# Optimization experiments

Hardware: AMD Instinct MI355X
Metric: run time of the kernel (lower is better)

Reference implementation:

```python
import jax, jax.numpy as jnp
import numpy as np

B, T, F, H = 512, 365, 16, 256


def _lstm_layer(x, W_ih, W_hh, b_ih, b_hh):
    """batch_first LSTM layer, torch gate order (i, f, g, o).
    x: [B, T, in]. Returns (outputs [B, T, H], final h [B, H])."""
    # Precompute input projections for all timesteps: [T, B, 4H]
    x_proj = jnp.einsum('bti,gi->tbg', x, W_ih) + (b_ih + b_hh)
    h0 = jnp.zeros((x.shape[0], W_hh.shape[1]), x.dtype)
    c0 = jnp.zeros_like(h0)

    def step(carry, xp):
        h, c = carry
        z = xp + h @ W_hh.T  # [B, 4H]
        i, f, g, o = jnp.split(z, 4, axis=-1)
        c = jax.nn.sigmoid(f) * c + jax.nn.sigmoid(i) * jnp.tanh(g)
        h = jax.nn.sigmoid(o) * jnp.tanh(c)
        return (h, c), h

    (hT, _), hs = jax.lax.scan(step, (h0, c0), x_proj)
    return jnp.transpose(hs, (1, 0, 2)), hT


def setup_inputs() -> dict:
    key = jax.random.key(0)
    ks = jax.random.split(key, 11)
    s1 = 1.0 / np.sqrt(H)
    u = lambda k, shape: jax.random.uniform(k, shape, jnp.float32, -s1, s1)
    return {
        'x': jax.random.normal(ks[0], (B, T, F), jnp.float32),
        'W_ih1': u(ks[1], (4 * H, F)),
        'W_hh1': u(ks[2], (4 * H, H)),
        'b_ih1': u(ks[3], (4 * H,)),
        'b_hh1': u(ks[4], (4 * H,)),
        'W_ih2': u(ks[5], (4 * H, H)),
        'W_hh2': u(ks[6], (4 * H, H)),
        'b_ih2': u(ks[7], (4 * H,)),
        'b_hh2': u(ks[8], (4 * H,)),
        'W_lin': u(ks[9], (1, H)),
        'b_lin': u(ks[10], (1,)),
    }


def reference(x, W_ih1, W_hh1, b_ih1, b_hh1, W_ih2, W_hh2, b_ih2, b_hh2, W_lin, b_lin):
    h1_seq, _ = _lstm_layer(x, W_ih1, W_hh1, b_ih1, b_hh1)
    # dropout(p=0.1) is identity in eval mode
    _, hT = _lstm_layer(h1_seq, W_ih2, W_hh2, b_ih2, b_hh2)
    out = (hT @ W_lin.T + b_lin).reshape(-1)  # [B]
    return out
```

## Files before the change

kernel.cpp:

```cpp
#include <hip/hip_runtime.h>


#define T_STEPS 365
#define RS 564

typedef __attribute__((ext_vector_type(8))) short short8;
typedef __attribute__((ext_vector_type(4))) float float4_;
typedef __attribute__((ext_vector_type(4))) unsigned int uint4_;
typedef unsigned long long u64;
typedef unsigned int u32;

#define MFMA16(a, b, c) __builtin_amdgcn_mfma_f32_16x16x32_bf16((a), (b), (c), 0, 0, 0)

__device__ __forceinline__ unsigned short f2bf(float v) {
    union { float f; u32 u; } a; a.f = v;
    u32 r = a.u + 0x7fffu + ((a.u >> 16) & 1u);
    return (unsigned short)(r >> 16);
}
__device__ __forceinline__ float bf2f(unsigned short h) {
    union { u32 u; float f; } a; a.u = ((u32)h) << 16; return a.f;
}
__device__ __forceinline__ u32 packhl(float v) {
    unsigned short hi = f2bf(v);
    unsigned short lo = f2bf(v - bf2f(hi));
    return ((u32)hi << 16) | (u32)lo;
}
__device__ __forceinline__ float sigm(float x)  { return 1.f / (1.f + __expf(-x)); }
__device__ __forceinline__ float tanh_(float x) { return 2.f / (1.f + __expf(-2.f * x)) - 1.f; }

__device__ __forceinline__ void unpk(uint4_ a, uint4_ b, short8& hi, short8& lo) {
    union U { u32 d[4]; short8 s; } H, L;
    H.d[0] = __builtin_amdgcn_perm(a.y, a.x, 0x07060302u);
    H.d[1] = __builtin_amdgcn_perm(a.w, a.z, 0x07060302u);
    H.d[2] = __builtin_amdgcn_perm(b.y, b.x, 0x07060302u);
    H.d[3] = __builtin_amdgcn_perm(b.w, b.z, 0x07060302u);
    L.d[0] = __builtin_amdgcn_perm(a.y, a.x, 0x05040100u);
    L.d[1] = __builtin_amdgcn_perm(a.w, a.z, 0x05040100u);
    L.d[2] = __builtin_amdgcn_perm(b.y, b.x, 0x05040100u);
    L.d[3] = __builtin_amdgcn_perm(b.w, b.z, 0x05040100u);
    hi = H.s; lo = L.s;
}

__global__ void prep_w(
    const float* __restrict__ Wih1, const float* __restrict__ Whh1,
    const float* __restrict__ bih1, const float* __restrict__ bhh1,
    const float* __restrict__ Wih2, const float* __restrict__ Whh2,
    const float* __restrict__ bih2, const float* __restrict__ bhh2,
    unsigned short* __restrict__ w1h, unsigned short* __restrict__ w1l,
    unsigned short* __restrict__ w2h, unsigned short* __restrict__ w2l,
    float* __restrict__ bias1, float* __restrict__ bias2)
{
    const int tile = blockIdx.x;
    const int g = tile >> 4, ns = tile & 15;
    const int tid = threadIdx.x;

    for (int idx = tid; idx < 9 * 512; idx += 256) {
        int ks = idx >> 9, off = idx & 511, r = off >> 5, kk = off & 31;
        int R = g * 256 + ns * 16 + r;
        float v;
        if (ks < 8)       v = Whh1[R * 256 + ks * 32 + kk];
        else if (kk < 16) v = Wih1[R * 16 + kk];
        else              v = 0.f;
        unsigned short h = f2bf(v);
        size_t d = (size_t)(tile * 9 + ks) * 512 + off;
        w1h[d] = h; w1l[d] = f2bf(v - bf2f(h));
    }
    for (int idx = tid; idx < 16 * 512; idx += 256) {
        int ks = idx >> 9, off = idx & 511, r = off >> 5, kk = off & 31;
        int R = g * 256 + ns * 16 + r;
        int k = ks * 32 + kk;
        float v = (k < 256) ? Wih2[R * 256 + k] : Whh2[R * 256 + (k - 256)];
        unsigned short h = f2bf(v);
        size_t d = (size_t)(tile * 16 + ks) * 512 + off;
        w2h[d] = h; w2l[d] = f2bf(v - bf2f(h));
    }
    if (tid < 16) {
        int R = g * 256 + ns * 16 + tid;
        bias1[R] = bih1[R] + bhh1[R];
        bias2[R] = bih2[R] + bhh2[R];
    }
}

__global__ __launch_bounds__(512, 2) void lstm_main(
    const float* __restrict__ x,
    const unsigned short* __restrict__ w1h, const unsigned short* __restrict__ w1l,
    const unsigned short* __restrict__ w2h, const unsigned short* __restrict__ w2l,
    const float* __restrict__ bias1, const float* __restrict__ bias2,
    u32* hb1, u32* hb2, u32* prog,
    const float* __restrict__ Wlin, const float* __restrict__ blin,
    float* __restrict__ out)
{
    __shared__ __align__(16) u32 A2u[32 * RS];
    __shared__ __align__(16) float zb1[3 * 64 * 36];
    __shared__ __align__(16) float zb2[5 * 64 * 36];
    __shared__ __align__(16) float hp[32][17];
    __shared__ u32 rdy;

    const int tid  = threadIdx.x;
    const int lane = tid & 63;
    const int wv   = tid >> 6;
    const int quad = lane >> 4;
    const int r16  = lane & 15;
    const int bg   = blockIdx.x & 15;
    const int ns   = blockIdx.x >> 4;

    u32* myprog = prog + bg * 256;

    const bool isL1 = (wv < 3);
    int t0, t1_, t2_, t3_;
    if      (wv == 0) { t0 = 0;  t1_ = 1;  t2_ = 2;  t3_ = -1; }
    else if (wv == 1) { t0 = 3;  t1_ = 4;  t2_ = 5;  t3_ = -1; }
    else if (wv == 2) { t0 = 6;  t1_ = 7;  t2_ = 8;  t3_ = -1; }
    else if (wv == 3) { t0 = 0;  t1_ = 1;  t2_ = 2;  t3_ = 3;  }
    else if (wv == 4) { t0 = 4;  t1_ = 5;  t2_ = 6;  t3_ = -1; }
    else if (wv == 5) { t0 = 7;  t1_ = 9;  t2_ = 10; t3_ = -1; }
    else if (wv == 6) { t0 = 11; t1_ = 12; t2_ = 13; t3_ = -1; }
    else              { t0 = 14; t1_ = 15; t2_ = 16; t3_ = -1; }

    const int loff = r16 * 32 + quad * 8;
    const unsigned short* WHsrc = isL1 ? w1h : w2h;
    const unsigned short* WLsrc = isL1 ? w1l : w2l;
    const int NK = isL1 ? 9 : 16;
    short8 WH[4][4], WL[4][4];
#pragma unroll
    for (int s = 0; s < 4; s++) {
        const int b = (s == 0) ? t0 : (s == 1) ? t1_ : (s == 2) ? t2_ : t3_;
#pragma unroll
        for (int g = 0; g < 4; g++) {
            if (b >= 0) {
                int ks = (!isL1 && b > 8) ? (b - 1) : b;
                size_t off = ((size_t)((g * 16 + ns) * NK + ks)) * 512 + loff;
                WH[g][s] = *(const short8*)(WHsrc + off);
                WL[g][s] = *(const short8*)(WLsrc + off);
            } else {
                WH[g][s] = short8{0,0,0,0,0,0,0,0};
                WL[g][s] = short8{0,0,0,0,0,0,0,0};
            }
        }
    }

    float bi[4] = {0.f, 0.f, 0.f, 0.f};
    if (tid < 256) {
        const float* bsrc = (tid < 128) ? bias1 : bias2;
        int colg = ns * 16 + (tid & 15);
#pragma unroll
        for (int g = 0; g < 4; g++) bi[g] = bsrc[g * 256 + colg];
    }
    float cst[4] = {0.f, 0.f, 0.f, 0.f};

    for (int i = tid; i < 32 * RS; i += 512) A2u[i] = 0u;
    if (tid == 0) rdy = 0u;
    __syncthreads();
    {
        int row = tid >> 4, col = tid & 15;
        float v = x[((size_t)(bg * 32 + row) * T_STEPS + 0) * 16 + col];
        A2u[row * RS + 256 + col] = packhl(v);
    }
    __syncthreads();

    for (int t = 0; t <= T_STEPS; t++) {
        const int p = t & 1;

        float4_ acc[4][2];
        const float4_ z4 = {0.f, 0.f, 0.f, 0.f};
#pragma unroll
        for (int g = 0; g < 4; g++) { acc[g][0] = z4; acc[g][1] = z4; }

#pragma unroll
        for (int s = 0; s < 4; s++) {
            const int b = (s == 0) ? t0 : (s == 1) ? t1_ : (s == 2) ? t2_ : t3_;
            if (b >= 0) {
                const int base0 = r16 * RS + b * 32 + quad * 8;
                uint4_ p00 = *(const uint4_*)&A2u[base0];
                uint4_ p01 = *(const uint4_*)&A2u[base0 + 4];
                uint4_ p10 = *(const uint4_*)&A2u[base0 + 16 * RS];
                uint4_ p11 = *(const uint4_*)&A2u[base0 + 16 * RS + 4];
                short8 ah0, al0, ah1, al1;
                unpk(p00, p01, ah0, al0);
                unpk(p10, p11, ah1, al1);
#pragma unroll
                for (int g = 0; g < 4; g++) {
                    acc[g][0] = MFMA16(ah0, WH[g][s], acc[g][0]);
                    acc[g][0] = MFMA16(al0, WH[g][s], acc[g][0]);
                    acc[g][0] = MFMA16(ah0, WL[g][s], acc[g][0]);
                    acc[g][1] = MFMA16(ah1, WH[g][s], acc[g][1]);
                    acc[g][1] = MFMA16(al1, WH[g][s], acc[g][1]);
                    acc[g][1] = MFMA16(ah1, WL[g][s], acc[g][1]);
                }
            }
        }
        {
            float* zbase = isL1 ? (zb1 + wv * (64 * 36)) : (zb2 + (wv - 3) * (64 * 36));
#pragma unroll
            for (int g = 0; g < 4; g++)
#pragma unroll
                for (int rt = 0; rt < 2; rt++)
                    *(float4_*)&zbase[(size_t)(g * 16 + r16) * 36 + rt * 16 + quad * 4] = acc[g][rt];
        }
        __syncthreads();

        if (tid < 256) {
            const bool is1 = (tid < 128);
            const int hcol = tid & 15;
            const int rq   = (tid >> 4) & 7;
            const float* zb = is1 ? zb1 : zb2;
            const int np = is1 ? 3 : 5;
            float4_ z[4];
#pragma unroll
            for (int g = 0; g < 4; g++) {
                float4_ s = {bi[g], bi[g], bi[g], bi[g]};
#pragma unroll
                for (int pw = 0; pw < 5; pw++) {
                    if (pw < np)
                        s += *(const float4_*)&zb[(size_t)(pw * 64 + g * 16 + hcol) * 36 + rq * 4];
                }
                z[g] = s;
            }
            u32* hb = is1 ? hb1 : hb2;
            const int slot = is1 ? p : (1 - p);
            size_t o = (((size_t)slot * 16 + bg) * 32 + rq * 4) * 256 + ns * 16 + hcol;
#pragma unroll
            for (int j = 0; j < 4; j++) {
                float zi = z[0][j], zf = z[1][j], zg = z[2][j], zo = z[3][j];
                float nc = sigm(zf) * cst[j] + sigm(zi) * tanh_(zg);
                float h  = sigm(zo) * tanh_(nc);
                if (!is1 && t == 0) { nc = 0.f; h = 0.f; }
                cst[j] = nc;
                __hip_atomic_store(&hb[o + (size_t)j * 256], packhl(h),
                                   __ATOMIC_RELAXED, __HIP_MEMORY_SCOPE_WORKGROUP);
            }
            asm volatile("s_waitcnt vmcnt(0)" ::: "memory");
            if (lane == 0)
                __hip_atomic_store(&myprog[ns * 16 + wv], (u32)(t + 1),
                                   __ATOMIC_RELAXED, __HIP_MEMORY_SCOPE_WORKGROUP);
        } else {
            const int i0 = tid - 256;
            const int tn = (t + 1 <= T_STEPS - 1) ? (t + 1) : (T_STEPS - 1);
#pragma unroll
            for (int k = 0; k < 2; k++) {
                int idx = i0 + 256 * k;
                int row = idx >> 4, col = idx & 15;
                float v = x[((size_t)(bg * 32 + row) * T_STEPS + tn) * 16 + col];
                A2u[row * RS + 256 + col] = packhl(v);
            }
        }

        if (t == T_STEPS) break;

        {
            const u32 tgt = (u32)(t + 1);
            if (wv == 7) {
                const int fidx = (lane >> 2) * 16 + (lane & 3);
                while (__hip_atomic_load(&myprog[fidx], __ATOMIC_RELAXED,
                                         __HIP_MEMORY_SCOPE_AGENT) < tgt)
                    __builtin_amdgcn_s_sleep(1);
                if (lane == 0)
                    __hip_atomic_store(&rdy, tgt, __ATOMIC_RELEASE,
                                       __HIP_MEMORY_SCOPE_WORKGROUP);
            } else {
                while (__hip_atomic_load(&rdy, __ATOMIC_ACQUIRE,
                                         __HIP_MEMORY_SCOPE_WORKGROUP) < tgt) {}
            }
        }

        {
            const u64* s1 = (const u64*)(hb1 + (size_t)(p * 16 + bg) * 32 * 256);
            const u64* s2 = (const u64*)(hb2 + (size_t)((1 - p) * 16 + bg) * 32 * 256);
#pragma unroll
            for (int j = 0; j < 4; j++) {
                const int row = wv * 4 + j;
                const u64* r1 = s1 + (size_t)row * 128;
                const u64* r2 = s2 + (size_t)row * 128;
                u64 a = __hip_atomic_load(r1 + lane,      __ATOMIC_RELAXED, __HIP_MEMORY_SCOPE_AGENT);
                u64 b = __hip_atomic_load(r1 + 64 + lane, __ATOMIC_RELAXED, __HIP_MEMORY_SCOPE_AGENT);
                u64 c = __hip_atomic_load(r2 + lane,      __ATOMIC_RELAXED, __HIP_MEMORY_SCOPE_AGENT);
                u64 d = __hip_atomic_load(r2 + 64 + lane, __ATOMIC_RELAXED, __HIP_MEMORY_SCOPE_AGENT);
                u32* dst = &A2u[row * RS];
                *(u64*)&dst[2 * lane]             = a;
                *(u64*)&dst[128 + 2 * lane]       = b;
                *(u64*)&dst[288 + 2 * lane]       = c;
                *(u64*)&dst[288 + 128 + 2 * lane] = d;
            }
        }
        __syncthreads();
    }

    if (ns != 0) return;
    {
        const u32 tgt = (u32)(T_STEPS + 1);
        const int fidx = (lane >> 2) * 16 + (lane & 3);
        while (__hip_atomic_load(&myprog[fidx], __ATOMIC_RELAXED,
                                 __HIP_MEMORY_SCOPE_AGENT) < tgt)
            __builtin_amdgcn_s_sleep(1);
    }
    {
        int row = tid >> 4, seg = tid & 15;
        const u32* src = hb2 + ((size_t)bg * 32 + row) * 256 + seg * 16;
        float s = 0.f;
#pragma unroll
        for (int j = 0; j < 16; j++) {
            u32 v = __hip_atomic_load(&src[j], __ATOMIC_RELAXED, __HIP_MEMORY_SCOPE_AGENT);
            s += (bf2f((unsigned short)(v >> 16)) + bf2f((unsigned short)v)) * Wlin[seg * 16 + j];
        }
        hp[row][seg] = s;
    }
    __syncthreads();
    if (tid < 32) {
        float s = 0.f;
#pragma unroll
        for (int j = 0; j < 16; j++) s += hp[tid][j];
        out[bg * 32 + tid] = s + blin[0];
    }
}

extern "C" void kernel_launch(void* const* d_in, const int* in_sizes, int n_in,
                              void* d_out, int out_size, void* d_ws, size_t ws_size,
                              hipStream_t stream) {
    const float* x    = (const float*)d_in[0];
    const float* Wih1 = (const float*)d_in[1];
    const float* Whh1 = (const float*)d_in[2];
    const float* bih1 = (const float*)d_in[3];
    const float* bhh1 = (const float*)d_in[4];
    const float* Wih2 = (const float*)d_in[5];
    const float* Whh2 = (const float*)d_in[6];
    const float* bih2 = (const float*)d_in[7];
    const float* bhh2 = (const float*)d_in[8];
    const float* Wlin = (const float*)d_in[9];
    const float* blin = (const float*)d_in[10];
    float* out = (float*)d_out;

    char* pp = (char*)d_ws;
    unsigned short* w1h = (unsigned short*)pp; pp += (size_t)64 * 9 * 512 * 2;
    unsigned short* w1l = (unsigned short*)pp; pp += (size_t)64 * 9 * 512 * 2;
    unsigned short* w2h = (unsigned short*)pp; pp += (size_t)64 * 16 * 512 * 2;
    unsigned short* w2l = (unsigned short*)pp; pp += (size_t)64 * 16 * 512 * 2;
    float* bias1 = (float*)pp; pp += 1024 * 4;
    float* bias2 = (float*)pp; pp += 1024 * 4;
    char* zero_base = pp;
    u32* hb1 = (u32*)pp; pp += (size_t)2 * 16 * 32 * 256 * 4;
    u32* hb2 = (u32*)pp; pp += (size_t)2 * 16 * 32 * 256 * 4;
    u32* prog = (u32*)pp; pp += 16 * 256 * 4;
    size_t zero_bytes = (size_t)(pp - zero_base);

    hipMemsetAsync(zero_base, 0, zero_bytes, stream);
    prep_w<<<64, 256, 0, stream>>>(Wih1, Whh1, bih1, bhh1, Wih2, Whh2, bih2, bhh2,
                                   w1h, w1l, w2h, w2l, bias1, bias2);
    lstm_main<<<256, 512, 0, stream>>>(x, w1h, w1l, w2h, w2l, bias1, bias2,
                                       hb1, hb2, prog, Wlin, blin, out);
}
```

Before: 1.663 ms.

## Spread LSTM gate elementwise work across all 8 waves and prefetch x earlier

The gate nonlinearity and cell update now run on all 512 threads, each handling 2 batch rows instead of 4, rather than only the first 256 threads. The next-step x load is issued before the z-buffer stores and the barrier, and is written into LDS afterwards. The MFMA block is wrapped in s_setprio to raise wave priority. Because all 8 waves now publish progress flags, the wave-7 spin waits check twice as many flags. The aim is to shorten the serial elementwise phase on each timestep's critical path, at the cost of more progress-flag polling.

Result: no change. 1.634 ms (median of 2 runs) (-1.8%).

```diff
diff --git a/kernel.cpp b/kernel.cpp
--- a/kernel.cpp
+++ b/kernel.cpp
@@ -6,6 +6,7 @@
 
 typedef __attribute__((ext_vector_type(8))) short short8;
 typedef __attribute__((ext_vector_type(4))) float float4_;
+typedef __attribute__((ext_vector_type(2))) float float2_;
 typedef __attribute__((ext_vector_type(4))) unsigned int uint4_;
 typedef unsigned long long u64;
 typedef unsigned int u32;
@@ -139,22 +140,26 @@
         }
     }
 
-    float bi[4] = {0.f, 0.f, 0.f, 0.f};
-    if (tid < 256) {
-        const float* bsrc = (tid < 128) ? bias1 : bias2;
-        int colg = ns * 16 + (tid & 15);
+    const bool is1u = (tid < 256);
+    const int hcol = tid & 15;
+    const int qrp  = (tid >> 4) & 15;
+    float bi[4];
+    {
+        const float* bsrc = is1u ? bias1 : bias2;
+        int colg = ns * 16 + hcol;
 #pragma unroll
         for (int g = 0; g < 4; g++) bi[g] = bsrc[g * 256 + colg];
     }
-    float cst[4] = {0.f, 0.f, 0.f, 0.f};
+    float cA = 0.f, cB = 0.f;
+
+    const int xrow = tid >> 4, xcol = tid & 15;
 
     for (int i = tid; i < 32 * RS; i += 512) A2u[i] = 0u;
     if (tid == 0) rdy = 0u;
     __syncthreads();
     {
-        int row = tid >> 4, col = tid & 15;
-        float v = x[((size_t)(bg * 32 + row) * T_STEPS + 0) * 16 + col];
-        A2u[row * RS + 256 + col] = packhl(v);
+        float v = x[((size_t)(bg * 32 + xrow) * T_STEPS + 0) * 16 + xcol];
+        A2u[xrow * RS + 256 + xcol] = packhl(v);
     }
     __syncthreads();
 
@@ -166,6 +171,7 @@
 #pragma unroll
         for (int g = 0; g < 4; g++) { acc[g][0] = z4; acc[g][1] = z4; }
 
+        __builtin_amdgcn_s_setprio(1);
 #pragma unroll
         for (int s = 0; s < 4; s++) {
             const int b = (s == 0) ? t0 : (s == 1) ? t1_ : (s == 2) ? t2_ : t3_;
@@ -189,6 +195,14 @@
                 }
             }
         }
+        __builtin_amdgcn_s_setprio(0);
+
+        float xval;
+        {
+            const int tn = (t + 1 <= T_STEPS - 1) ? (t + 1) : (T_STEPS - 1);
+            xval = x[((size_t)(bg * 32 + xrow) * T_STEPS + tn) * 16 + xcol];
+        }
+
         {
             float* zbase = isL1 ? (zb1 + wv * (64 * 36)) : (zb2 + (wv - 3) * (64 * 36));
 #pragma unroll
@@ -199,50 +213,47 @@
         }
         __syncthreads();
 
-        if (tid < 256) {
-            const bool is1 = (tid < 128);
-            const int hcol = tid & 15;
-            const int rq   = (tid >> 4) & 7;
-            const float* zb = is1 ? zb1 : zb2;
-            const int np = is1 ? 3 : 5;
-            float4_ z[4];
+        {
+            A2u[xrow * RS + 256 + xcol] = packhl(xval);
+
+            const float* zb = is1u ? zb1 : zb2;
+            const int np = is1u ? 3 : 5;
+            float z0[4], z1[4];
 #pragma unroll
             for (int g = 0; g < 4; g++) {
-                float4_ s = {bi[g], bi[g], bi[g], bi[g]};
+                float s0 = bi[g], s1 = bi[g];
 #pragma unroll
                 for (int pw = 0; pw < 5; pw++) {
-                    if (pw < np)
-                        s += *(const float4_*)&zb[(size_t)(pw * 64 + g * 16 + hcol) * 36 + rq * 4];
+                    if (pw < np) {
+                        float2_ v = *(const float2_*)&zb[(size_t)(pw * 64 + g * 16 + hcol) * 36 + 2 * qrp];
+                        s0 += v.x; s1 += v.y;
+                    }
                 }
-                z[g] = s;
-            }
-            u32* hb = is1 ? hb1 : hb2;
-            const int slot = is1 ? p : (1 - p);
-            size_t o = (((size_t)slot * 16 + bg) * 32 + rq * 4) * 256 + ns * 16 + hcol;
-#pragma unroll
-            for (int j = 0; j < 4; j++) {
-                float zi = z[0][j], zf = z[1][j], zg = z[2][j], zo = z[3][j];
-                float nc = sigm(zf) * cst[j] + sigm(zi) * tanh_(zg);
-                float h  = sigm(zo) * tanh_(nc);
-                if (!is1 && t == 0) { nc = 0.f; h = 0.f; }
-                cst[j] = nc;
-                __hip_atomic_store(&hb[o + (size_t)j * 256], packhl(h),
+                z0[g] = s0; z1[g] = s1;
+            }
+            u32* hb = is1u ? hb1 : hb2;
+            const int slot = is1u ? p : (1 - p);
+            size_t o = (((size_t)slot * 16 + bg) * 32 + 2 * qrp) * 256 + ns * 16 + hcol;
+            {
+                float nc = sigm(z0[1]) * cA + sigm(z0[0]) * tanh_(z0[2]);
+                float h  = sigm(z0[3]) * tanh_(nc);
+                if (!is1u && t == 0) { nc = 0.f; h = 0.f; }
+                cA = nc;
+                __hip_atomic_store(&hb[o], packhl(h),
+                                   __ATOMIC_RELAXED, __HIP_MEMORY_SCOPE_WORKGROUP);
+            }
+            {
+                float nc = sigm(z1[1]) * cB + sigm(z1[0]) * tanh_(z1[2]);
+                float h  = sigm(z1[3]) * tanh_(nc);
+                if (!is1u && t == 0) { nc = 0.f; h = 0.f; }
+                cB = nc;
+                __hip_atomic_store(&hb[o + 256], packhl(h),
                                    __ATOMIC_RELAXED, __HIP_MEMORY_SCOPE_WORKGROUP);
             }
             asm volatile("s_waitcnt vmcnt(0)" ::: "memory");
             if (lane == 0)
                 __hip_atomic_store(&myprog[ns * 16 + wv], (u32)(t + 1),
                                    __ATOMIC_RELAXED, __HIP_MEMORY_SCOPE_WORKGROUP);
-        } else {
-            const int i0 = tid - 256;
-            const int tn = (t + 1 <= T_STEPS - 1) ? (t + 1) : (T_STEPS - 1);
-#pragma unroll
-            for (int k = 0; k < 2; k++) {
-                int idx = i0 + 256 * k;
-                int row = idx >> 4, col = idx & 15;
-                float v = x[((size_t)(bg * 32 + row) * T_STEPS + tn) * 16 + col];
-                A2u[row * RS + 256 + col] = packhl(v);
-            }
         }
 
         if (t == T_STEPS) break;
@@ -250,10 +261,16 @@
         {
             const u32 tgt = (u32)(t + 1);
             if (wv == 7) {
-                const int fidx = (lane >> 2) * 16 + (lane & 3);
-                while (__hip_atomic_load(&myprog[fidx], __ATOMIC_RELAXED,
-                                         __HIP_MEMORY_SCOPE_AGENT) < tgt)
+                const int f1 = (lane >> 2) * 16 + (lane & 3);
+                const int f2 = f1 + 4;
+                for (;;) {
+                    u32 a = __hip_atomic_load(&myprog[f1], __ATOMIC_RELAXED,
+                                              __HIP_MEMORY_SCOPE_AGENT);
+                    u32 b = __hip_atomic_load(&myprog[f2], __ATOMIC_RELAXED,
+                                              __HIP_MEMORY_SCOPE_AGENT);
+                    if (a >= tgt && b >= tgt) break;
                     __builtin_amdgcn_s_sleep(1);
+                }
                 if (lane == 0)
                     __hip_atomic_store(&rdy, tgt, __ATOMIC_RELEASE,
                                        __HIP_MEMORY_SCOPE_WORKGROUP);
@@ -288,10 +305,16 @@
     if (ns != 0) return;
     {
         const u32 tgt = (u32)(T_STEPS + 1);
-        const int fidx = (lane >> 2) * 16 + (lane & 3);
-        while (__hip_atomic_load(&myprog[fidx], __ATOMIC_RELAXED,
-                                 __HIP_MEMORY_SCOPE_AGENT) < tgt)
+        const int f1 = (lane >> 2) * 16 + (lane & 3);
+        const int f2 = f1 + 4;
+        for (;;) {
+            u32 a = __hip_atomic_load(&myprog[f1], __ATOMIC_RELAXED,
+                                      __HIP_MEMORY_SCOPE_AGENT);
+            u32 b = __hip_atomic_load(&myprog[f2], __ATOMIC_RELAXED,
+                                      __HIP_MEMORY_SCOPE_AGENT);
+            if (a >= tgt && b >= tgt) break;
             __builtin_amdgcn_s_sleep(1);
+        }
     }
     {
         int row = tid >> 4, seg = tid & 15;
```
